# Performance work log

Measured on AMD Instinct MI355X. Metric: run time of the kernel, lower is better.

The kernel has to match this reference:

```python
import jax, jax.numpy as jnp
import numpy as np

N = 8192
E = 262144
NEG = 0.2  # leaky_relu negative slope used throughout


def setup_inputs() -> dict:
    key = jax.random.key(0)
    def rn(i, shape, s=0.05):
        return jax.random.normal(jax.random.fold_in(key, i), shape, jnp.float32) * s
    d = {}
    d["x"] = jax.random.normal(jax.random.fold_in(key, 0), (N, 64), jnp.float32)
    d["edge_index"] = jax.random.randint(jax.random.fold_in(key, 1), (2, E), 0, N, dtype=jnp.int32)
    wshapes = {"w0": (64, 256), "as0": (4, 64), "ad0": (4, 64), "r0": (64, 256),
               "w1": (256, 256), "as1": (4, 64), "ad1": (4, 64), "r1": (256, 256),
               "w2": (256, 64), "as2": (1, 64), "ad2": (1, 64), "r2": (256, 64),
               "p0": (256, 64), "p1": (256, 64),
               "qw": (64, 64), "kw": (64, 64), "vw": (64, 64), "ow": (64, 64),
               "m1w": (64, 64), "m2w": (64, 32), "m3w": (32, 10)}
    for i, (nm, sh) in enumerate(wshapes.items()):
        d[nm] = rn(i + 2, sh)
    for nm, dim in [("g0", 256), ("g1", 256), ("g2", 64)]:
        d[nm] = jnp.ones((dim,), jnp.float32)
    for nm, dim in [("be0", 256), ("be1", 256), ("be2", 64), ("b0", 256), ("b1", 256), ("b2", 64),
                    ("qb", 64), ("kb", 64), ("vb", 64), ("ob", 64), ("m1b", 64), ("m2b", 32), ("m3b", 10)]:
        d[nm] = jnp.zeros((dim,), jnp.float32)
    return d


def _forward(edge_index, x, w0, as0, ad0, b0, g0, be0, r0,
             w1, as1, ad1, b1, g1, be1, r1,
             w2, as2, ad2, b2, g2, be2, r2,
             p0, p1, qw, qb, kw, kb, vw, vb, ow, ob,
             m1w, m1b, m2w, m2b, m3w, m3b):
    n = x.shape[0]
    loops = jnp.arange(n, dtype=edge_index.dtype)
    src = jnp.concatenate([edge_index[0], loops])  # add_self_loops=True
    dst = jnp.concatenate([edge_index[1], loops])

    def gat(h, w, a_s, a_d, b, heads):
        hw = (h @ w).reshape(n, heads, 64)  # [N, H, C]
        # PyG GATConv: e_ij = leaky_relu(att_src . h_j + att_dst . h_i), softmax over in-edges of i
        e = jax.nn.leaky_relu(jnp.sum(hw * a_s, -1)[src] + jnp.sum(hw * a_d, -1)[dst], NEG)  # [Etot, H]
        m = jax.ops.segment_max(e, dst, num_segments=n)
        ex = jnp.exp(e - m[dst])
        den = jax.ops.segment_sum(ex, dst, num_segments=n)
        alpha = ex / (den[dst] + 1e-16)
        out = jax.ops.segment_sum(hw[src] * alpha[:, :, None], dst, num_segments=n)
        return out.reshape(n, heads * 64) + b

    def bn(h, g, bta):  # BatchNorm1d, batch statistics (training-mode math)
        mu = jnp.mean(h, 0)
        var = jnp.var(h, 0)
        return (h - mu) * jax.lax.rsqrt(var + 1e-5) * g + bta

    outs = []
    h = x
    for (w, a_s, a_d, b, g, bt, r, heads) in [
            (w0, as0, ad0, b0, g0, be0, r0, 4),
            (w1, as1, ad1, b1, g1, be1, r1, 4),
            (w2, as2, ad2, b2, g2, be2, r2, 1)]:
        res = h @ r
        h = bn(gat(h, w, a_s, a_d, b, heads), g, bt) + res  # shapes always match here
        h = jax.nn.leaky_relu(h, NEG)
        outs.append(h)

    # JumpingKnowledge 'max' after projecting first two layers to hidden dim
    z = jnp.maximum(jnp.maximum(outs[0] @ p0, outs[1] @ p1), outs[2])  # [N, 64]

    # MultiHeadSelfAttention over all nodes (batch=1 implicit), 2 heads, head_dim=32
    q = (z @ qw + qb).reshape(n, 2, 32)
    k = (z @ kw + kb).reshape(n, 2, 32)
    v = (z @ vw + vb).reshape(n, 2, 32)
    attn = jax.nn.softmax(jnp.einsum('nhd,mhd->hnm', q, k) * (32 ** -0.5), axis=-1)
    z = jnp.einsum('hnm,mhd->nhd', attn, v).reshape(n, 64) @ ow + ob

    # MLP head (no data.batch -> GlobalAttention pool skipped)
    z = jax.nn.leaky_relu(z @ m1w + m1b, NEG)
    z = jax.nn.leaky_relu(z @ m2w + m2b, NEG)
    return z @ m3w + m3b


def reference(x, edge_index, w0, as0, ad0, b0, g0, be0, r0,
              w1, as1, ad1, b1, g1, be1, r1,
              w2, as2, ad2, b2, g2, be2, r2,
              p0, p1, qw, qb, kw, kb, vw, vb, ow, ob,
              m1w, m1b, m2w, m2b, m3w, m3b):
    return _forward(edge_index, x, w0, as0, ad0, b0, g0, be0, r0,
                    w1, as1, ad1, b1, g1, be1, r1,
                    w2, as2, ad2, b2, g2, be2, r2,
                    p0, p1, qw, qb, kw, kb, vw, vb, ow, ob,
                    m1w, m1b, m2w, m2b, m3w, m3b)
```

## Files before the change

kernel.cpp:

```cpp
#include <hip/hip_runtime.h>
#include <hip/hip_bf16.h>


#define NEG 0.2f
#define LOG2E 1.4426950408889634f

__device__ __forceinline__ float leaky(float v) { return v > 0.f ? v : NEG * v; }

__device__ __forceinline__ unsigned bf16u(float x) {
    unsigned u = __float_as_uint(x);
    u += 0x7FFFu + ((u >> 16) & 1u);
    return u >> 16;
}
__device__ __forceinline__ unsigned fmap(float f) {
    unsigned u = __float_as_uint(f);
    return (u & 0x80000000u) ? ~u : (u | 0x80000000u);
}
__device__ __forceinline__ float funmap(unsigned u) {
    unsigned b = (u & 0x80000000u) ? (u & 0x7FFFFFFFu) : ~u;
    return __uint_as_float(b);
}
__device__ __forceinline__ float fexp2(float x) {
#if __has_builtin(__builtin_amdgcn_exp2f)
    return __builtin_amdgcn_exp2f(x);
#else
    return exp2f(x);
#endif
}
__device__ __forceinline__ unsigned cvtpk(float lo, float hi) {
    unsigned r;
    asm("v_cvt_pk_bf16_f32 %0, %1, %2" : "=v"(r) : "v"(lo), "v"(hi));
    return r;
}

typedef __attribute__((ext_vector_type(8))) short bf16x8;
typedef __attribute__((ext_vector_type(16))) float f32x16;
typedef __attribute__((ext_vector_type(4))) unsigned uint4v;

__device__ __forceinline__ void split1(float v, unsigned& hb, unsigned& lb) {
    hb = bf16u(v);
    float hf = __uint_as_float(hb << 16);
    lb = bf16u(v - hf);
}

__global__ void split_rows(const float* __restrict__ in,
                           unsigned short* __restrict__ hi,
                           unsigned short* __restrict__ lo, int total4)
{
    int i = blockIdx.x * 256 + threadIdx.x;
    if (i >= total4) return;
    float4 v = ((const float4*)in)[i];
    float vv[4] = {v.x, v.y, v.z, v.w};
    ushort4 h, l;
#pragma unroll
    for (int j = 0; j < 4; ++j) {
        unsigned hb, lb;
        split1(vv[j], hb, lb);
        (&h.x)[j] = (unsigned short)hb;
        (&l.x)[j] = (unsigned short)lb;
    }
    ((ushort4*)hi)[i] = h;
    ((ushort4*)lo)[i] = l;
}

struct WEnt { const float* src; unsigned short* hi; unsigned short* lo; int K; int N; };
struct WArr { WEnt e[15]; };

__global__ void split_weights(WArr a)
{
    WEnt w = a.e[blockIdx.y];
    int id = blockIdx.x * 256 + threadIdx.x;
    if (id >= w.K * w.N) return;
    int k = id / w.N, n = id - k * w.N;
    unsigned hb, lb;
    split1(w.src[id], hb, lb);
    w.hi[(size_t)n * w.K + k] = (unsigned short)hb;
    w.lo[(size_t)n * w.K + k] = (unsigned short)lb;
}

__global__ __launch_bounds__(256) void gemm_mfma(
    const unsigned short* __restrict__ Ahi, const unsigned short* __restrict__ Alo,
    const unsigned short* __restrict__ Bhi, const unsigned short* __restrict__ Blo,
    const float* __restrict__ bias, float* __restrict__ C,
    unsigned short* __restrict__ Chi, unsigned short* __restrict__ Clo,
    const float* __restrict__ jkB, const float* __restrict__ jkC,
    unsigned* __restrict__ kmaxDst, const float* __restrict__ kbias,
    int M, int N, int K, int act)
{
    const int lane = threadIdx.x & 63, wid = threadIdx.x >> 6;
    const int hb4 = lane >> 5, lq = lane & 31;
    const int row0 = blockIdx.y * 64 + (wid >> 1) * 32;
    const int col0 = blockIdx.x * 64 + (wid & 1) * 32;
    const size_t abase = (size_t)(row0 + lq) * K + hb4 * 8;
    const size_t bbase = (size_t)(col0 + lq) * K + hb4 * 8;
    f32x16 acc0, acc1;
#pragma unroll
    for (int r = 0; r < 16; ++r) { acc0[r] = 0.f; acc1[r] = 0.f; }
    for (int k0 = 0; k0 < K; k0 += 16) {
        bf16x8 a_h = *(const bf16x8*)(Ahi + abase + k0);
        bf16x8 a_l = *(const bf16x8*)(Alo + abase + k0);
        bf16x8 b_h = *(const bf16x8*)(Bhi + bbase + k0);
        bf16x8 b_l = *(const bf16x8*)(Blo + bbase + k0);
        acc0 = __builtin_amdgcn_mfma_f32_32x32x16_bf16(a_h, b_h, acc0, 0, 0, 0);
        acc1 = __builtin_amdgcn_mfma_f32_32x32x16_bf16(a_l, b_h, acc1, 0, 0, 0);
        acc1 = __builtin_amdgcn_mfma_f32_32x32x16_bf16(a_h, b_l, acc1, 0, 0, 0);
    }
    int col = col0 + lq;
    if (col >= N) return;
    float bs = bias ? bias[col] : 0.f;
    float kmx = 0.f;
#pragma unroll
    for (int r = 0; r < 16; ++r) {
        int row = row0 + (r & 3) + 8 * (r >> 2) + 4 * hb4;
        float v = acc0[r] + acc1[r] + bs;
        if (act) v = leaky(v);
        if (jkB) v = fmaxf(fmaxf(v, jkB[(size_t)row * N + col]),
                           jkC[(size_t)row * N + col]);
        if (kmaxDst) kmx = fmaxf(kmx, fabsf(v + kbias[col & 63]));
        if (C) C[(size_t)row * N + col] = v;
        if (Chi) {
            unsigned hh, ll;
            split1(v, hh, ll);
            Chi[(size_t)row * N + col] = (unsigned short)hh;
            Clo[(size_t)row * N + col] = (unsigned short)ll;
        }
    }
    if (kmaxDst && col >= 64 && col < 128)
        atomicMax(&kmaxDst[col - 64], __float_as_uint(kmx));
}

template <int H>
__global__ __launch_bounds__(256) void sd_kernel(
    const float* __restrict__ hwres, int S,
    const float* __restrict__ a_s, const float* __restrict__ a_d,
    float* __restrict__ sval, float* __restrict__ dval,
    unsigned* __restrict__ svmax, int Nn)
{
    int i = blockIdx.x * 256 + threadIdx.x;
    int n = i / H, h = i & (H - 1);
    const float4* row = (const float4*)(hwres + (size_t)n * S + h * 64);
    const float4* as4 = (const float4*)(a_s + h * 64);
    const float4* ad4 = (const float4*)(a_d + h * 64);
    float s = 0.f, d = 0.f;
#pragma unroll
    for (int c = 0; c < 16; ++c) {
        float4 x = row[c], a = as4[c], b = ad4[c];
        s += x.x * a.x + x.y * a.y + x.z * a.z + x.w * a.w;
        d += x.x * b.x + x.y * b.y + x.z * b.z + x.w * b.w;
    }
    s *= LOG2E;
    d *= LOG2E;
    sval[i] = s;
    dval[i] = d;
    float m = s;
#pragma unroll
    for (int off = H; off < 64; off <<= 1) m = fmaxf(m, __shfl_xor(m, off));
    if ((threadIdx.x & 63) < H) atomicMax(&svmax[h], fmap(m));
}

__global__ void csr_count(const int* __restrict__ ei, int* __restrict__ cnt, int E) {
    int i = blockIdx.x * 256 + threadIdx.x;
    if (i < E) atomicAdd(&cnt[ei[E + i]], 1);
}

__global__ __launch_bounds__(256) void csr_scan(const int* __restrict__ cnt,
                                                int* __restrict__ rowptr,
                                                int* __restrict__ fill, int Nn)
{
    __shared__ int part[256];
    int t = threadIdx.x;
    int loc[32];
    int s = 0;
#pragma unroll
    for (int j = 0; j < 32; ++j) { loc[j] = s; s += cnt[t * 32 + j]; }
    part[t] = s;
    __syncthreads();
    for (int d = 1; d < 256; d <<= 1) {
        int v = (t >= d) ? part[t - d] : 0;
        __syncthreads();
        part[t] += v;
        __syncthreads();
    }
    int off = (t > 0) ? part[t - 1] : 0;
#pragma unroll
    for (int j = 0; j < 32; ++j) {
        int v = off + loc[j];
        rowptr[t * 32 + j] = v;
        fill[t * 32 + j] = v;
    }
    if (t == 255) rowptr[Nn] = part[255];
}

__global__ void csr_scatter(const int* __restrict__ ei, int* __restrict__ fill,
                            int* __restrict__ srcidx, int E) {
    int i = blockIdx.x * 256 + threadIdx.x;
    if (i < E) {
        int d = ei[E + i];
        int p = atomicAdd(&fill[d], 1);
        srcidx[p] = ei[i];
    }
}

__global__ __launch_bounds__(256) void gat_gather4(
    const int* __restrict__ rowptr, const int* __restrict__ srcidx,
    const float* __restrict__ hwres, int S,
    const float* __restrict__ sval, const float* __restrict__ dval,
    const unsigned* __restrict__ svmax, float* __restrict__ gout, int Nn)
{
    const int node = blockIdx.x * 4 + (threadIdx.x >> 6);
    const int lane = threadIdx.x & 63;
    const int hd = lane >> 4;
    const int cb = lane * 4;
    const int beg = rowptr[node], end = rowptr[node + 1];
    const float dv = dval[node * 4 + hd];
    const float B = leaky(funmap(svmax[hd]) + dv);
    float p = fexp2(leaky(sval[node * 4 + hd] + dv) - B);
    float l = p;
    float4 hv = *(const float4*)(hwres + (size_t)node * S + cb);
    float a0 = p * hv.x, a1 = p * hv.y, a2 = p * hv.z, a3 = p * hv.w;
    int i = beg;
    for (; i + 2 <= end; i += 2) {
        int s0 = srcidx[i], s1 = srcidx[i + 1];
        float p0 = fexp2(leaky(sval[s0 * 4 + hd] + dv) - B);
        float p1 = fexp2(leaky(sval[s1 * 4 + hd] + dv) - B);
        float4 r0 = *(const float4*)(hwres + (size_t)s0 * S + cb);
        float4 r1 = *(const float4*)(hwres + (size_t)s1 * S + cb);
        l += p0 + p1;
        a0 += p0 * r0.x + p1 * r1.x;
        a1 += p0 * r0.y + p1 * r1.y;
        a2 += p0 * r0.z + p1 * r1.z;
        a3 += p0 * r0.w + p1 * r1.w;
    }
    if (i < end) {
        int s0 = srcidx[i];
        float p0 = fexp2(leaky(sval[s0 * 4 + hd] + dv) - B);
        float4 r0 = *(const float4*)(hwres + (size_t)s0 * S + cb);
        l += p0;
        a0 += p0 * r0.x; a1 += p0 * r0.y; a2 += p0 * r0.z; a3 += p0 * r0.w;
    }
    float inv = 1.f / l;
    *(float4*)(gout + (size_t)node * 256 + cb) =
        make_float4(a0 * inv, a1 * inv, a2 * inv, a3 * inv);
}

__global__ __launch_bounds__(256) void gat_gather1(
    const int* __restrict__ rowptr, const int* __restrict__ srcidx,
    const float* __restrict__ hwres, int S,
    const float* __restrict__ sval, const float* __restrict__ dval,
    const unsigned* __restrict__ svmax, float* __restrict__ gout, int Nn)
{
    const int node = blockIdx.x * 4 + (threadIdx.x >> 6);
    const int lane = threadIdx.x & 63;
    const int beg = rowptr[node], end = rowptr[node + 1];
    const float dv = dval[node];
    const float B = leaky(funmap(svmax[0]) + dv);
    float p = fexp2(leaky(sval[node] + dv) - B);
    float l = p;
    float acc = p * hwres[(size_t)node * S + lane];
    int i = beg;
    for (; i + 2 <= end; i += 2) {
        int s0 = srcidx[i], s1 = srcidx[i + 1];
        float p0 = fexp2(leaky(sval[s0] + dv) - B);
        float p1 = fexp2(leaky(sval[s1] + dv) - B);
        l += p0 + p1;
        acc += p0 * hwres[(size_t)s0 * S + lane] + p1 * hwres[(size_t)s1 * S + lane];
    }
    if (i < end) {
        int s0 = srcidx[i];
        float p0 = fexp2(leaky(sval[s0] + dv) - B);
        l += p0;
        acc += p0 * hwres[(size_t)s0 * S + lane];
    }
    gout[(size_t)node * 64 + lane] = acc / l;
}

__global__ void bn_partial(const float* __restrict__ gout, double* __restrict__ sums,
                           int Nn, int C)
{
    int t = threadIdx.x;
    int c = t % C, sub = t / C, nsub = blockDim.x / C;
    int rbase = blockIdx.x * 32;
    double s = 0.0, sq = 0.0;
    for (int r = rbase + sub; r < rbase + 32; r += nsub) {
        float x = gout[(size_t)r * C + c];
        s += x;
        sq += (double)x * x;
    }
    atomicAdd(&sums[c], s);
    atomicAdd(&sums[C + c], sq);
}

__global__ void bn_res_act(const float* __restrict__ gout,
                           const float* __restrict__ hwres, int S, int logC,
                           const double* __restrict__ bnsum, double invN,
                           const float* __restrict__ g, const float* __restrict__ be,
                           float* __restrict__ outp,
                           unsigned short* __restrict__ shi,
                           unsigned short* __restrict__ slo, int total)
{
    int i = blockIdx.x * blockDim.x + threadIdx.x;
    if (i >= total) return;
    int C = 1 << logC;
    int c = i & (C - 1), row = i >> logC;
    double m = bnsum[c] * invN;
    double var = bnsum[C + c] * invN - m * m;
    float mu = (float)m;
    float rstd = (float)(1.0 / sqrt(var + 1e-5));
    float v = (gout[i] - mu) * rstd * g[c] + be[c]
              + hwres[(size_t)row * S + C + c];
    v = leaky(v);
    if (outp) outp[i] = v;
    if (shi) {
        unsigned hb, lb;
        split1(v, hb, lb);
        shi[i] = (unsigned short)hb;
        slo[i] = (unsigned short)lb;
    }
}

__global__ void qkv_prep(const float* __restrict__ zqkv,
                         const float* __restrict__ qb, const float* __restrict__ kb,
                         const float* __restrict__ vb,
                         const unsigned* __restrict__ kmaxu,
                         __hip_bfloat16* __restrict__ Qb, __hip_bfloat16* __restrict__ Kb,
                         __hip_bfloat16* __restrict__ Vf, float* __restrict__ bound,
                         int N)
{
    int idx = blockIdx.x * 256 + threadIdx.x;
    if (idx < 2 * N) {
        int h = idx / N, row = idx - h * N;
        const float scale = 0.17677669529663687f * LOG2E;
        const float* qp = zqkv + (size_t)row * 192 + h * 32;
        const float* kp = zqkv + (size_t)row * 192 + 64 + h * 32;
        float b = 0.f;
        unsigned qo[16], ko[16];
#pragma unroll
        for (int i = 0; i < 16; ++i) {
            float q0 = (qp[2 * i] + qb[h * 32 + 2 * i]) * scale;
            float q1 = (qp[2 * i + 1] + qb[h * 32 + 2 * i + 1]) * scale;
            float k0 = kp[2 * i] + kb[h * 32 + 2 * i];
            float k1 = kp[2 * i + 1] + kb[h * 32 + 2 * i + 1];
            b += fabsf(q0) * __uint_as_float(kmaxu[h * 32 + 2 * i]);
            b += fabsf(q1) * __uint_as_float(kmaxu[h * 32 + 2 * i + 1]);
            qo[i] = bf16u(q0) | (bf16u(q1) << 16);
            ko[i] = bf16u(k0) | (bf16u(k1) << 16);
        }
        uint4* qd = (uint4*)(Qb + (size_t)idx * 32);
        uint4* kd = (uint4*)(Kb + (size_t)idx * 32);
#pragma unroll
        for (int i = 0; i < 4; ++i) {
            qd[i] = make_uint4(qo[4 * i], qo[4 * i + 1], qo[4 * i + 2], qo[4 * i + 3]);
            kd[i] = make_uint4(ko[4 * i], ko[4 * i + 1], ko[4 * i + 2], ko[4 * i + 3]);
        }
        bound[idx] = b;
    } else {
        int j = idx - 2 * N;
        if (j >= 2 * (N >> 4) * 64) return;
        int lane = j & 63;
        int g = (j >> 6) % (N >> 4);
        int h = (j >> 6) / (N >> 4);
        int hi = lane >> 5;
        int kbase = g * 16 + 4 * hi;
        int d = (lane & 31) + h * 32;
        float bd = vb[d];
        unsigned o[4];
#pragma unroll
        for (int i = 0; i < 4; ++i) {
            int r0 = kbase + ((2 * i) & 3) + 8 * (i >> 1);
            unsigned u0 = bf16u(zqkv[(size_t)r0 * 192 + 128 + d] + bd);
            unsigned u1 = bf16u(zqkv[(size_t)(r0 + 1) * 192 + 128 + d] + bd);
            o[i] = u0 | (u1 << 16);
        }
        *(uint4*)(Vf + (size_t)j * 8) = make_uint4(o[0], o[1], o[2], o[3]);
    }
}

__global__ __launch_bounds__(256) void attn_mfma(
    const __hip_bfloat16* __restrict__ Qb, const __hip_bfloat16* __restrict__ Kb,
    const __hip_bfloat16* __restrict__ Vf, const float* __restrict__ bound,
    float* __restrict__ pl, __hip_bfloat16* __restrict__ pacc,
    int N, int nchunk, int chunksz)
{
    const int lane = threadIdx.x & 63;
    const int wid = threadIdx.x >> 6;
    const int hi = lane >> 5, lq = lane & 31;
    const int chunk = blockIdx.x;
    const int qtile = blockIdx.y * 4 + wid;
    const int head = qtile / (N >> 5);
    const int q0 = (qtile % (N >> 5)) * 32;
    const int kbase = chunk * chunksz;

    const size_t qrow = (size_t)head * N + q0 + lq;
    const bf16x8 qf0 = *(const bf16x8*)(Qb + qrow * 32 + hi * 8);
    const bf16x8 qf1 = *(const bf16x8*)(Qb + qrow * 32 + hi * 8 + 16);
    const float bnd = bound[qrow];

    f32x16 oacc;
#pragma unroll
    for (int r = 0; r < 16; ++r) oacc[r] = 0.f;
    float lsum = 0.f;

    for (int kt = kbase; kt < kbase + chunksz; kt += 32) {
        const size_t krow = (size_t)head * N + kt + lq;
        const bf16x8 kf0 = *(const bf16x8*)(Kb + krow * 32 + hi * 8);
        const bf16x8 kf1 = *(const bf16x8*)(Kb + krow * 32 + hi * 8 + 16);
        f32x16 s;
#pragma unroll
        for (int r = 0; r < 16; ++r) s[r] = 0.f;
        s = __builtin_amdgcn_mfma_f32_32x32x16_bf16(kf0, qf0, s, 0, 0, 0);
        s = __builtin_amdgcn_mfma_f32_32x32x16_bf16(kf1, qf1, s, 0, 0, 0);
        const __hip_bfloat16* vfb =
            Vf + (((size_t)head * (N >> 4) + (kt >> 4)) * 64 + lane) * 8;
        const bf16x8 vf0 = *(const bf16x8*)vfb;
        const bf16x8 vf1 = *(const bf16x8*)(vfb + 64 * 8);

        float p[16];
#pragma unroll
        for (int r = 0; r < 16; ++r) p[r] = fexp2(s[r] - bnd);
        float ls = 0.f;
#pragma unroll
        for (int r = 0; r < 16; ++r) ls += p[r];
        lsum += ls;

        uint4v b1, b2;
        b1[0] = cvtpk(p[0], p[1]);
        b1[1] = cvtpk(p[2], p[3]);
        b1[2] = cvtpk(p[4], p[5]);
        b1[3] = cvtpk(p[6], p[7]);
        b2[0] = cvtpk(p[8], p[9]);
        b2[1] = cvtpk(p[10], p[11]);
        b2[2] = cvtpk(p[12], p[13]);
        b2[3] = cvtpk(p[14], p[15]);
        oacc = __builtin_amdgcn_mfma_f32_32x32x16_bf16(
            vf0, __builtin_bit_cast(bf16x8, b1), oacc, 0, 0, 0);
        oacc = __builtin_amdgcn_mfma_f32_32x32x16_bf16(
            vf1, __builtin_bit_cast(bf16x8, b2), oacc, 0, 0, 0);
    }
    lsum += __shfl_xor(lsum, 32);
    const size_t hr = (size_t)head * N + q0 + lq;
    if (hi == 0) pl[hr * nchunk + chunk] = lsum;
    __hip_bfloat16* pb = pacc + (hr * nchunk + chunk) * 32;
#pragma unroll
    for (int rg = 0; rg < 4; ++rg) {
        unsigned lo = cvtpk(oacc[rg * 4 + 0], oacc[rg * 4 + 1]);
        unsigned hw2 = cvtpk(oacc[rg * 4 + 2], oacc[rg * 4 + 3]);
        *(uint2*)(pb + rg * 8 + hi * 4) = make_uint2(lo, hw2);
    }
}

__global__ __launch_bounds__(256) void mlp_fused(
    const float* __restrict__ pl, const __hip_bfloat16* __restrict__ pacc,
    const unsigned short* __restrict__ Owh, const unsigned short* __restrict__ Owl,
    const float* __restrict__ ob,
    const unsigned short* __restrict__ M1h, const unsigned short* __restrict__ M1l,
    const float* __restrict__ m1b,
    const unsigned short* __restrict__ M2h, const unsigned short* __restrict__ M2l,
    const float* __restrict__ m2b,
    const unsigned short* __restrict__ M3h, const unsigned short* __restrict__ M3l,
    const float* __restrict__ m3b,
    float* __restrict__ out, int N, int nchunk)
{
    __shared__ __align__(16) unsigned short Shi[64][72];
    __shared__ __align__(16) unsigned short Slo[64][72];
    const int t = threadIdx.x;
    const int row0 = blockIdx.x * 64;
#pragma unroll
    for (int i = 0; i < 16; ++i) {
        int idx = i * 256 + t;
        int row = idx >> 6, ch = idx & 63;
        int head = ch >> 5, cc = ch & 31;
        size_t hr = (size_t)head * N + row0 + row;
        float l = 0.f, a = 0.f;
        for (int c = 0; c < nchunk; ++c) {
            l += pl[hr * nchunk + c];
            a += __bfloat162float(pacc[(hr * nchunk + c) * 32 + cc]);
        }
        float v = a / l;
        unsigned hb, lb;
        split1(v, hb, lb);
        Shi[row][ch] = (unsigned short)hb;
        Slo[row][ch] = (unsigned short)lb;
    }
    __syncthreads();

    const int lane = t & 63, wid = t >> 6;
    const int hb4 = lane >> 5, lq = lane & 31;
    const int rowb = (wid >> 1) * 32, colb = (wid & 1) * 32;
    const unsigned short* Wh[4] = {Owh, M1h, M2h, M3h};
    const unsigned short* Wl[4] = {Owl, M1l, M2l, M3l};
    const float* Wb[4] = {ob, m1b, m2b, m3b};
    const int Ncs[4] = {64, 64, 32, 10};
    const int Kcs[4] = {64, 64, 64, 32};
    const int actf[4] = {0, 1, 1, 0};

#pragma unroll
    for (int s = 0; s < 4; ++s) {
        const int Nc = Ncs[s], K = Kcs[s];
        const int col = colb + lq;
        const bool active = colb < Nc;
        f32x16 acc0, acc1;
#pragma unroll
        for (int r = 0; r < 16; ++r) { acc0[r] = 0.f; acc1[r] = 0.f; }
        if (active) {
            for (int k0 = 0; k0 < K; k0 += 16) {
                bf16x8 a_h = *(const bf16x8*)&Shi[rowb + lq][k0 + hb4 * 8];
                bf16x8 a_l = *(const bf16x8*)&Slo[rowb + lq][k0 + hb4 * 8];
                bf16x8 b_h = *(const bf16x8*)&Wh[s][(size_t)col * K + k0 + hb4 * 8];
                bf16x8 b_l = *(const bf16x8*)&Wl[s][(size_t)col * K + k0 + hb4 * 8];
                acc0 = __builtin_amdgcn_mfma_f32_32x32x16_bf16(a_h, b_h, acc0, 0, 0, 0);
                acc1 = __builtin_amdgcn_mfma_f32_32x32x16_bf16(a_l, b_h, acc1, 0, 0, 0);
                acc1 = __builtin_amdgcn_mfma_f32_32x32x16_bf16(a_h, b_l, acc1, 0, 0, 0);
            }
        }
        __syncthreads();
        if (s == 3) {
            if (active && col < 10) {
#pragma unroll
                for (int r = 0; r < 16; ++r) {
                    int row = rowb + (r & 3) + 8 * (r >> 2) + 4 * hb4;
                    out[(size_t)(row0 + row) * 10 + col] =
                        acc0[r] + acc1[r] + m3b[col];
                }
            }
        } else {
            if (active) {
                float bs = Wb[s][col];
#pragma unroll
                for (int r = 0; r < 16; ++r) {
                    int row = rowb + (r & 3) + 8 * (r >> 2) + 4 * hb4;
                    float v = acc0[r] + acc1[r] + bs;
                    if (actf[s]) v = leaky(v);
                    unsigned hb, lb;
                    split1(v, hb, lb);
                    Shi[row][col] = (unsigned short)hb;
                    Slo[row][col] = (unsigned short)lb;
                }
            }
            __syncthreads();
        }
    }
}

extern "C" void kernel_launch(void* const* d_in, const int* in_sizes, int n_in,
                              void* d_out, int out_size, void* d_ws, size_t ws_size,
                              hipStream_t stream)
{
    const float* x = (const float*)d_in[0];
    const int* ei = (const int*)d_in[1];
    const float* w[3]   = {(const float*)d_in[2], (const float*)d_in[6],  (const float*)d_in[10]};
    const float* as_[3] = {(const float*)d_in[3], (const float*)d_in[7],  (const float*)d_in[11]};
    const float* ad_[3] = {(const float*)d_in[4], (const float*)d_in[8],  (const float*)d_in[12]};
    const float* rw[3]  = {(const float*)d_in[5], (const float*)d_in[9],  (const float*)d_in[13]};
    const float* p0 = (const float*)d_in[14];
    const float* p1 = (const float*)d_in[15];
    const float* qw = (const float*)d_in[16];
    const float* kw = (const float*)d_in[17];
    const float* vw = (const float*)d_in[18];
    const float* ow = (const float*)d_in[19];
    const float* m1w = (const float*)d_in[20];
    const float* m2w = (const float*)d_in[21];
    const float* m3w = (const float*)d_in[22];
    const float* g_[3]  = {(const float*)d_in[23], (const float*)d_in[24], (const float*)d_in[25]};
    const float* be_[3] = {(const float*)d_in[26], (const float*)d_in[27], (const float*)d_in[28]};
    const float* qb  = (const float*)d_in[32];
    const float* kb  = (const float*)d_in[33];
    const float* vb  = (const float*)d_in[34];
    const float* ob  = (const float*)d_in[35];
    const float* m1b = (const float*)d_in[36];
    const float* m2b = (const float*)d_in[37];
    const float* m3b = (const float*)d_in[38];

    const int N = in_sizes[0] / 64;
    const int E = in_sizes[1] / 2;

    float* ws = (float*)d_ws;
    size_t off = 0;
    auto alloc = [&](size_t n) {
        float* p = ws + off;
        off += (n + 255) & ~(size_t)255;
        return p;
    };
    float* hwres = alloc((size_t)N * 512);
    float* gout  = alloc((size_t)N * 256);
    unsigned short* sChi = (unsigned short*)alloc((size_t)N * 128);
    unsigned short* sClo = (unsigned short*)alloc((size_t)N * 128);
    float* h2   = alloc((size_t)N * 64);
    float* sval = alloc((size_t)N * 4);
    float* dval = alloc((size_t)N * 4);
    size_t ms_begin = off;
    int* cnt = (int*)alloc(N);
    double* bnsum = (double*)alloc(3 * 1024);
    unsigned* kmaxu = (unsigned*)alloc(64);
    unsigned* svmax = (unsigned*)alloc(16);
    size_t ms_end = off;
    int* rowptr = (int*)alloc(N + 256);
    int* fill   = (int*)alloc(N);
    int* srcidx = (int*)alloc(E);
    unsigned short* sAhi = (unsigned short*)alloc((size_t)N * 128);
    unsigned short* sAlo = (unsigned short*)alloc((size_t)N * 128);
    unsigned short* sBhi = (unsigned short*)alloc((size_t)N * 32);
    unsigned short* sBlo = (unsigned short*)alloc((size_t)N * 32);
    unsigned short* G0h = (unsigned short*)alloc(512 * 64 / 2);
    unsigned short* G0l = (unsigned short*)alloc(512 * 64 / 2);
    unsigned short* G1h = (unsigned short*)alloc(512 * 256 / 2);
    unsigned short* G1l = (unsigned short*)alloc(512 * 256 / 2);
    unsigned short* G2h = (unsigned short*)alloc(128 * 256 / 2);
    unsigned short* G2l = (unsigned short*)alloc(128 * 256 / 2);
    unsigned short* P0h = (unsigned short*)alloc(64 * 256 / 2);
    unsigned short* P0l = (unsigned short*)alloc(64 * 256 / 2);
    unsigned short* P1h = (unsigned short*)alloc(64 * 256 / 2);
    unsigned short* P1l = (unsigned short*)alloc(64 * 256 / 2);
    unsigned short* Gqh = (unsigned short*)alloc(192 * 64 / 2);
    unsigned short* Gql = (unsigned short*)alloc(192 * 64 / 2);
    unsigned short* Owh = (unsigned short*)alloc(64 * 64 / 2);
    unsigned short* Owl = (unsigned short*)alloc(64 * 64 / 2);
    unsigned short* M1h = (unsigned short*)alloc(64 * 64 / 2);
    unsigned short* M1l = (unsigned short*)alloc(64 * 64 / 2);
    unsigned short* M2h = (unsigned short*)alloc(64 * 64 / 2);
    unsigned short* M2l = (unsigned short*)alloc(64 * 64 / 2);
    unsigned short* M3h = (unsigned short*)alloc(64 * 32 / 2);
    unsigned short* M3l = (unsigned short*)alloc(64 * 32 / 2);
    float* zqkv = hwres;
    __hip_bfloat16* pacc = (__hip_bfloat16*)(hwres + (size_t)N * 192);
    float* tB = gout;
    const int NCHUNK = 8;
    __hip_bfloat16* Qb = (__hip_bfloat16*)sChi;
    __hip_bfloat16* Kb = Qb + (size_t)2 * N * 32;
    __hip_bfloat16* Vf = Kb + (size_t)2 * N * 32;
    float* boundArr = (float*)(Vf + (size_t)2 * N * 32);
    float* pl = h2;

    {
        WArr wa;
        wa.e[0]  = WEnt{w[0],  G0h,              G0l,              64, 256};
        wa.e[1]  = WEnt{rw[0], G0h + 256 * 64,   G0l + 256 * 64,   64, 256};
        wa.e[2]  = WEnt{w[1],  G1h,              G1l,              256, 256};
        wa.e[3]  = WEnt{rw[1], G1h + 256 * 256,  G1l + 256 * 256,  256, 256};
        wa.e[4]  = WEnt{w[2],  G2h,              G2l,              256, 64};
        wa.e[5]  = WEnt{rw[2], G2h + 64 * 256,   G2l + 64 * 256,   256, 64};
        wa.e[6]  = WEnt{p0,    P0h,              P0l,              256, 64};
        wa.e[7]  = WEnt{p1,    P1h,              P1l,              256, 64};
        wa.e[8]  = WEnt{qw,    Gqh,              Gql,              64, 64};
        wa.e[9]  = WEnt{kw,    Gqh + 64 * 64,    Gql + 64 * 64,    64, 64};
        wa.e[10] = WEnt{vw,    Gqh + 128 * 64,   Gql + 128 * 64,   64, 64};
        wa.e[11] = WEnt{ow,    Owh,              Owl,              64, 64};
        wa.e[12] = WEnt{m1w,   M1h,              M1l,              64, 64};
        wa.e[13] = WEnt{m2w,   M2h,              M2l,              64, 32};
        wa.e[14] = WEnt{m3w,   M3h,              M3l,              32, 10};
        split_weights<<<dim3(256, 15), 256, 0, stream>>>(wa);
    }
    hipMemsetAsync(ws + ms_begin, 0, (ms_end - ms_begin) * 4, stream);
    csr_count<<<(E + 255) / 256, 256, 0, stream>>>(ei, cnt, E);
    csr_scan<<<1, 256, 0, stream>>>(cnt, rowptr, fill, N);
    csr_scatter<<<(E + 255) / 256, 256, 0, stream>>>(ei, fill, srcidx, E);
    split_rows<<<(N * 64 / 4 + 255) / 256, 256, 0, stream>>>(x, sAhi, sAlo, N * 64 / 4);

    auto gemmM = [&](const unsigned short* Ah, const unsigned short* Al,
                     const unsigned short* Bh, const unsigned short* Bl,
                     const float* bias, float* C, unsigned short* Chi,
                     unsigned short* Clo, const float* jkB, const float* jkC,
                     unsigned* kmx, const float* kbias,
                     int M, int Nc, int K, int act) {
        dim3 grid((Nc + 63) / 64, M / 64);
        gemm_mfma<<<grid, 256, 0, stream>>>(Ah, Al, Bh, Bl, bias, C, Chi, Clo,
                                            jkB, jkC, kmx, kbias, M, Nc, K, act);
    };

    const unsigned short* inh[3] = {sAhi, sChi, sAhi};
    const unsigned short* inl[3] = {sAlo, sClo, sAlo};
    unsigned short* outh[3] = {sChi, sAhi, nullptr};
    unsigned short* outl[3] = {sClo, sAlo, nullptr};
    const unsigned short* Gh[3] = {G0h, G1h, G2h};
    const unsigned short* Gl[3] = {G0l, G1l, G2l};
    int Ksz[3] = {64, 256, 256}, Csz[3] = {256, 256, 64}, logC[3] = {8, 8, 6};
    int Hh[3] = {4, 4, 1};

    for (int l = 0; l < 3; ++l) {
        int C = Csz[l], S = 2 * C;
        gemmM(inh[l], inl[l], Gh[l], Gl[l], nullptr, hwres, nullptr, nullptr,
              nullptr, nullptr, nullptr, nullptr, N, S, Ksz[l], 0);
        if (Hh[l] == 4) {
            sd_kernel<4><<<N * 4 / 256, 256, 0, stream>>>(
                hwres, S, as_[l], ad_[l], sval, dval, svmax + l * 4, N);
            gat_gather4<<<N / 4, 256, 0, stream>>>(
                rowptr, srcidx, hwres, S, sval, dval, svmax + l * 4, gout, N);
        } else {
            sd_kernel<1><<<N / 256, 256, 0, stream>>>(
                hwres, S, as_[l], ad_[l], sval, dval, svmax + l * 4, N);
            gat_gather1<<<N / 4, 256, 0, stream>>>(
                rowptr, srcidx, hwres, S, sval, dval, svmax + l * 4, gout, N);
        }
        double* bns = bnsum + l * 512;
        bn_partial<<<N / 32, 256, 0, stream>>>(gout, bns, N, C);
        bn_res_act<<<((size_t)N * C) / 256, 256, 0, stream>>>(
            gout, hwres, S, logC[l], bns, 1.0 / (double)N, g_[l], be_[l],
            l == 2 ? h2 : nullptr, outh[l], outl[l], N * C);
    }

    gemmM(sAhi, sAlo, P1h, P1l, nullptr, tB, nullptr, nullptr,
          nullptr, nullptr, nullptr, nullptr, N, 64, 256, 0);
    gemmM(sChi, sClo, P0h, P0l, nullptr, nullptr, sBhi, sBlo,
          tB, h2, nullptr, nullptr, N, 64, 256, 0);

    gemmM(sBhi, sBlo, Gqh, Gql, nullptr, zqkv, nullptr, nullptr,
          nullptr, nullptr, kmaxu, kb, N, 192, 64, 0);

    int ptot = 2 * N + 2 * (N >> 4) * 64;
    qkv_prep<<<(ptot + 255) / 256, 256, 0, stream>>>(
        zqkv, qb, kb, vb, kmaxu, Qb, Kb, Vf, boundArr, N);
    attn_mfma<<<dim3(NCHUNK, (2 * N / 32) / 4), 256, 0, stream>>>(
        Qb, Kb, Vf, boundArr, pl, pacc, N, NCHUNK, N / NCHUNK);

    mlp_fused<<<N / 64, 256, 0, stream>>>(
        pl, pacc, Owh, Owl, ob, M1h, M1l, m1b, M2h, M2l, m2b,
        M3h, M3l, m3b, (float*)d_out, N, NCHUNK);
}
```

Baseline: 403.1 us.

## Unroll GAT gather loops by four and split fused MLP into combine plus GEMMs

The GAT gather kernels now process four neighbours per iteration instead of two, so more independent loads are in flight, and the remainder is handled by a scalar loop. The fused attention-combine plus MLP kernel is replaced by a separate attn_combine kernel that writes split-bf16 activations to global memory, followed by four generic gemmM launches for the output projection and the three MLP layers. This trades the shared-memory fusion for extra launches and global round-trips. It may also simplify correctness or reuse the tuned GEMM path.

```diff
diff --git a/kernel.cpp b/kernel.cpp
--- a/kernel.cpp
+++ b/kernel.cpp
@@ -219,19 +219,24 @@
     float4 hv = *(const float4*)(hwres + (size_t)node * S + cb);
     float a0 = p * hv.x, a1 = p * hv.y, a2 = p * hv.z, a3 = p * hv.w;
     int i = beg;
-    for (; i + 2 <= end; i += 2) {
+    for (; i + 4 <= end; i += 4) {
         int s0 = srcidx[i], s1 = srcidx[i + 1];
+        int s2 = srcidx[i + 2], s3 = srcidx[i + 3];
         float p0 = fexp2(leaky(sval[s0 * 4 + hd] + dv) - B);
         float p1 = fexp2(leaky(sval[s1 * 4 + hd] + dv) - B);
+        float p2 = fexp2(leaky(sval[s2 * 4 + hd] + dv) - B);
+        float p3 = fexp2(leaky(sval[s3 * 4 + hd] + dv) - B);
         float4 r0 = *(const float4*)(hwres + (size_t)s0 * S + cb);
         float4 r1 = *(const float4*)(hwres + (size_t)s1 * S + cb);
-        l += p0 + p1;
-        a0 += p0 * r0.x + p1 * r1.x;
-        a1 += p0 * r0.y + p1 * r1.y;
-        a2 += p0 * r0.z + p1 * r1.z;
-        a3 += p0 * r0.w + p1 * r1.w;
-    }
-    if (i < end) {
+        float4 r2 = *(const float4*)(hwres + (size_t)s2 * S + cb);
+        float4 r3 = *(const float4*)(hwres + (size_t)s3 * S + cb);
+        l += (p0 + p1) + (p2 + p3);
+        a0 += p0 * r0.x + p1 * r1.x + p2 * r2.x + p3 * r3.x;
+        a1 += p0 * r0.y + p1 * r1.y + p2 * r2.y + p3 * r3.y;
+        a2 += p0 * r0.z + p1 * r1.z + p2 * r2.z + p3 * r3.z;
+        a3 += p0 * r0.w + p1 * r1.w + p2 * r2.w + p3 * r3.w;
+    }
+    for (; i < end; ++i) {
         int s0 = srcidx[i];
         float p0 = fexp2(leaky(sval[s0 * 4 + hd] + dv) - B);
         float4 r0 = *(const float4*)(hwres + (size_t)s0 * S + cb);
@@ -258,14 +263,18 @@
     float l = p;
     float acc = p * hwres[(size_t)node * S + lane];
     int i = beg;
-    for (; i + 2 <= end; i += 2) {
+    for (; i + 4 <= end; i += 4) {
         int s0 = srcidx[i], s1 = srcidx[i + 1];
+        int s2 = srcidx[i + 2], s3 = srcidx[i + 3];
         float p0 = fexp2(leaky(sval[s0] + dv) - B);
         float p1 = fexp2(leaky(sval[s1] + dv) - B);
-        l += p0 + p1;
-        acc += p0 * hwres[(size_t)s0 * S + lane] + p1 * hwres[(size_t)s1 * S + lane];
-    }
-    if (i < end) {
+        float p2 = fexp2(leaky(sval[s2] + dv) - B);
+        float p3 = fexp2(leaky(sval[s3] + dv) - B);
+        l += (p0 + p1) + (p2 + p3);
+        acc += p0 * hwres[(size_t)s0 * S + lane] + p1 * hwres[(size_t)s1 * S + lane]
+             + p2 * hwres[(size_t)s2 * S + lane] + p3 * hwres[(size_t)s3 * S + lane];
+    }
+    for (; i < end; ++i) {
         int s0 = srcidx[i];
         float p0 = fexp2(leaky(sval[s0] + dv) - B);
         l += p0;
@@ -448,97 +457,26 @@
     }
 }
 
-__global__ __launch_bounds__(256) void mlp_fused(
-    const float* __restrict__ pl, const __hip_bfloat16* __restrict__ pacc,
-    const unsigned short* __restrict__ Owh, const unsigned short* __restrict__ Owl,
-    const float* __restrict__ ob,
-    const unsigned short* __restrict__ M1h, const unsigned short* __restrict__ M1l,
-    const float* __restrict__ m1b,
-    const unsigned short* __restrict__ M2h, const unsigned short* __restrict__ M2l,
-    const float* __restrict__ m2b,
-    const unsigned short* __restrict__ M3h, const unsigned short* __restrict__ M3l,
-    const float* __restrict__ m3b,
-    float* __restrict__ out, int N, int nchunk)
-{
-    __shared__ __align__(16) unsigned short Shi[64][72];
-    __shared__ __align__(16) unsigned short Slo[64][72];
-    const int t = threadIdx.x;
-    const int row0 = blockIdx.x * 64;
-#pragma unroll
-    for (int i = 0; i < 16; ++i) {
-        int idx = i * 256 + t;
-        int row = idx >> 6, ch = idx & 63;
-        int head = ch >> 5, cc = ch & 31;
-        size_t hr = (size_t)head * N + row0 + row;
-        float l = 0.f, a = 0.f;
-        for (int c = 0; c < nchunk; ++c) {
-            l += pl[hr * nchunk + c];
-            a += __bfloat162float(pacc[(hr * nchunk + c) * 32 + cc]);
-        }
-        float v = a / l;
-        unsigned hb, lb;
-        split1(v, hb, lb);
-        Shi[row][ch] = (unsigned short)hb;
-        Slo[row][ch] = (unsigned short)lb;
-    }
-    __syncthreads();
-
-    const int lane = t & 63, wid = t >> 6;
-    const int hb4 = lane >> 5, lq = lane & 31;
-    const int rowb = (wid >> 1) * 32, colb = (wid & 1) * 32;
-    const unsigned short* Wh[4] = {Owh, M1h, M2h, M3h};
-    const unsigned short* Wl[4] = {Owl, M1l, M2l, M3l};
-    const float* Wb[4] = {ob, m1b, m2b, m3b};
-    const int Ncs[4] = {64, 64, 32, 10};
-    const int Kcs[4] = {64, 64, 64, 32};
-    const int actf[4] = {0, 1, 1, 0};
-
-#pragma unroll
-    for (int s = 0; s < 4; ++s) {
-        const int Nc = Ncs[s], K = Kcs[s];
-        const int col = colb + lq;
-        const bool active = colb < Nc;
-        f32x16 acc0, acc1;
-#pragma unroll
-        for (int r = 0; r < 16; ++r) { acc0[r] = 0.f; acc1[r] = 0.f; }
-        if (active) {
-            for (int k0 = 0; k0 < K; k0 += 16) {
-                bf16x8 a_h = *(const bf16x8*)&Shi[rowb + lq][k0 + hb4 * 8];
-                bf16x8 a_l = *(const bf16x8*)&Slo[rowb + lq][k0 + hb4 * 8];
-                bf16x8 b_h = *(const bf16x8*)&Wh[s][(size_t)col * K + k0 + hb4 * 8];
-                bf16x8 b_l = *(const bf16x8*)&Wl[s][(size_t)col * K + k0 + hb4 * 8];
-                acc0 = __builtin_amdgcn_mfma_f32_32x32x16_bf16(a_h, b_h, acc0, 0, 0, 0);
-                acc1 = __builtin_amdgcn_mfma_f32_32x32x16_bf16(a_l, b_h, acc1, 0, 0, 0);
-                acc1 = __builtin_amdgcn_mfma_f32_32x32x16_bf16(a_h, b_l, acc1, 0, 0, 0);
-            }
-        }
-        __syncthreads();
-        if (s == 3) {
-            if (active && col < 10) {
-#pragma unroll
-                for (int r = 0; r < 16; ++r) {
-                    int row = rowb + (r & 3) + 8 * (r >> 2) + 4 * hb4;
-                    out[(size_t)(row0 + row) * 10 + col] =
-                        acc0[r] + acc1[r] + m3b[col];
-                }
-            }
-        } else {
-            if (active) {
-                float bs = Wb[s][col];
-#pragma unroll
-                for (int r = 0; r < 16; ++r) {
-                    int row = rowb + (r & 3) + 8 * (r >> 2) + 4 * hb4;
-                    float v = acc0[r] + acc1[r] + bs;
-                    if (actf[s]) v = leaky(v);
-                    unsigned hb, lb;
-                    split1(v, hb, lb);
-                    Shi[row][col] = (unsigned short)hb;
-                    Slo[row][col] = (unsigned short)lb;
-                }
-            }
-            __syncthreads();
-        }
-    }
+__global__ void attn_combine(const float* __restrict__ pl,
+                             const __hip_bfloat16* __restrict__ pacc,
+                             unsigned short* __restrict__ shi,
+                             unsigned short* __restrict__ slo, int N, int nchunk)
+{
+    int i = blockIdx.x * blockDim.x + threadIdx.x;
+    if (i >= 2 * N * 32) return;
+    int hr = i >> 5, cc = i & 31;
+    float l = 0.f, a = 0.f;
+    for (int c = 0; c < nchunk; ++c) {
+        l += pl[(size_t)hr * nchunk + c];
+        a += __bfloat162float(pacc[((size_t)hr * nchunk + c) * 32 + cc]);
+    }
+    int head = hr / N, row = hr - head * N;
+    float v = a / l;
+    size_t oi = (size_t)row * 64 + head * 32 + cc;
+    unsigned hb, lb;
+    split1(v, hb, lb);
+    shi[oi] = (unsigned short)hb;
+    slo[oi] = (unsigned short)lb;
 }
 
 extern "C" void kernel_launch(void* const* d_in, const int* in_sizes, int n_in,
@@ -622,7 +560,8 @@
     unsigned short* M3l = (unsigned short*)alloc(64 * 32 / 2);
     float* zqkv = hwres;
     __hip_bfloat16* pacc = (__hip_bfloat16*)(hwres + (size_t)N * 192);
-    float* tB = gout;
+    float* tA = gout;
+    float* tB = gout + (size_t)N * 64;
     const int NCHUNK = 8;
     __hip_bfloat16* Qb = (__hip_bfloat16*)sChi;
     __hip_bfloat16* Kb = Qb + (size_t)2 * N * 32;
@@ -710,8 +649,15 @@
         zqkv, qb, kb, vb, kmaxu, Qb, Kb, Vf, boundArr, N);
     attn_mfma<<<dim3(NCHUNK, (2 * N / 32) / 4), 256, 0, stream>>>(
         Qb, Kb, Vf, boundArr, pl, pacc, N, NCHUNK, N / NCHUNK);
-
-    mlp_fused<<<N / 64, 256, 0, stream>>>(
-        pl, pacc, Owh, Owl, ob, M1h, M1l, m1b, M2h, M2l, m2b,
-        M3h, M3l, m3b, (float*)d_out, N, NCHUNK);
-}
+    attn_combine<<<(2 * N * 32 + 255) / 256, 256, 0, stream>>>(
+        pl, pacc, sAhi, sAlo, N, NCHUNK);
+
+    gemmM(sAhi, sAlo, Owh, Owl, ob, tA, sBhi, sBlo,
+          nullptr, nullptr, nullptr, nullptr, N, 64, 64, 0);
+    gemmM(sBhi, sBlo, M1h, M1l, m1b, nullptr, sAhi, sAlo,
+          nullptr, nullptr, nullptr, nullptr, N, 64, 64, 1);
+    gemmM(sAhi, sAlo, M2h, M2l, m2b, nullptr, sBhi, sBlo,
+          nullptr, nullptr, nullptr, nullptr, N, 32, 64, 1);
+    gemmM(sBhi, sBlo, M3h, M3l, m3b, (float*)d_out, nullptr, nullptr,
+          nullptr, nullptr, nullptr, nullptr, N, 10, 32, 0);
+}
```

After: 397.7 us. Within noise of the previous version (-1.3%).
